# Kernel tuning notes

Hardware: AMD Instinct MI355X
Metric: run time of the kernel (lower is better)

## Reference

```python
import jax, jax.numpy as jnp
import numpy as np

B, Q, C, H, NSTEPS = 1024, 96, 16, 100, 100  # batch, q (MA order), channels, hidden, Euler steps


def setup_inputs() -> dict:
    key = jax.random.key(0)
    ks = jax.random.split(key, 6)
    s = 0.1  # weight init scale
    return {
        "series": jax.random.normal(ks[0], (B, Q, C), jnp.float32),
        "rand_error": jax.random.normal(ks[1], (B, 1, C), jnp.float32),
        "W1": jax.random.normal(ks[2], (H, Q + 2), jnp.float32) * s,
        "b1": jnp.zeros((H,), jnp.float32),
        "W2": jax.random.normal(ks[3], (H, H), jnp.float32) * s,
        "b2": jnp.zeros((H,), jnp.float32),
        "W3": jax.random.normal(ks[4], (Q + 1, H), jnp.float32) * s,
        "b3": jnp.zeros((Q + 1,), jnp.float32),
    }


def _mlp(x, t, W1, b1, W2, b2, W3, b3):
    # x: (B, Q+1, C), t: (B, 1, C)  -> cat along feature dim, permute to (B, C, Q+2)
    inp = jnp.concatenate([x, t], axis=1).transpose(0, 2, 1)
    h = jnp.tanh(inp @ W1.T + b1)
    h = jnp.tanh(h @ W2.T + b2)
    out = h @ W3.T + b3            # (B, C, Q+1)
    return out.transpose(0, 2, 1)  # (B, Q+1, C)


def reference(series, rand_error, W1, b1, W2, b2, W3, b3):
    # ma_forecast sampling path: noise = cat(series, rand_error) then Euler flow sampling
    noise = jnp.concatenate([series, rand_error], axis=1)  # (B, Q+1, C)
    dt = jnp.float32(1.0 / NSTEPS)

    def step(x, i):
        t = jnp.ones((x.shape[0], 1, x.shape[2]), x.dtype) * (i.astype(x.dtype) / NSTEPS)
        pred = _mlp(x, t, W1, b1, W2, b2, W3, b3)
        return x + (pred - noise) * dt, None

    x, _ = jax.lax.scan(step, noise, jnp.arange(NSTEPS))
    return x
```

## Files before the change

### kernel.cpp

```cpp
#include <hip/hip_runtime.h>


#define NB 1024
#define NQ 96
#define NC 16
#define NH 100
#define QP1 97
#define QP2 98
#define NTHR 256
#define STR 136
#define NSTEPS_ 100
#define MT_K 128

typedef __attribute__((ext_vector_type(8))) short bf16x8;
typedef __attribute__((ext_vector_type(4))) float f32x4;
typedef __attribute__((ext_vector_type(2))) float f32x2;
typedef __attribute__((ext_vector_type(2))) unsigned uintx2;

#define LO2(v) __builtin_shufflevector(v, v, 0, 1)
#define HI2(v) __builtin_shufflevector(v, v, 2, 3)

__device__ __forceinline__ f32x4 splat4(float f) {
  f32x4 v = f;
  return v;
}

__device__ __forceinline__ f32x2 splat2(float f) {
  f32x2 v = f;
  return v;
}

__device__ __forceinline__ short f2bf_rne(float f) {
  unsigned u = __builtin_bit_cast(unsigned, f);
  u = u + 0x7fffu + ((u >> 16) & 1u);
  return (short)(u >> 16);
}

__device__ __forceinline__ unsigned cvtpk_bf16(float a, float b) {
  unsigned r;
  asm("v_cvt_pk_bf16_f32 %0, %1, %2" : "=v"(r) : "v"(a), "v"(b));
  return r;
}

__device__ __forceinline__ void tanh_pair(f32x2& p, f32x2& q) {
  f32x2 up = p * p, uq = q * q;
  f32x2 np = p * __builtin_elementwise_fma(up + splat2(105.0f), up, splat2(945.0f));
  f32x2 nq = q * __builtin_elementwise_fma(uq + splat2(105.0f), uq, splat2(945.0f));
  f32x2 dp = __builtin_elementwise_fma(
      __builtin_elementwise_fma(splat2(15.0f), up, splat2(420.0f)), up,
      splat2(945.0f));
  f32x2 dq = __builtin_elementwise_fma(
      __builtin_elementwise_fma(splat2(15.0f), uq, splat2(420.0f)), uq,
      splat2(945.0f));
  f32x2 rp, rq;
  rp[0] = __builtin_amdgcn_rcpf(dp[0]);
  rp[1] = __builtin_amdgcn_rcpf(dp[1]);
  rq[0] = __builtin_amdgcn_rcpf(dq[0]);
  rq[1] = __builtin_amdgcn_rcpf(dq[1]);
  f32x2 vp = np * rp, vq = nq * rq;
  p = __builtin_elementwise_min(
      __builtin_elementwise_max(vp, splat2(-1.0f)), splat2(1.0f));
  q = __builtin_elementwise_min(
      __builtin_elementwise_max(vq, splat2(-1.0f)), splat2(1.0f));
}

__global__ void __launch_bounds__(512) arima_prep(
    const float* __restrict__ W1, const float* __restrict__ b1,
    const float* __restrict__ W3, const float* __restrict__ b3,
    short* __restrict__ Mt, float* __restrict__ sv) {
  __shared__ float part[4][128];
  __shared__ float pb[128];
  const int n = blockIdx.x;
  const int tid = threadIdx.x;
  const int k = tid & 127, js = tid >> 7;
  float s = 0.0f;
  if (n < NH && k < NH) {
    int j0 = js * 25, j1 = (js == 3) ? QP1 : j0 + 25;
    for (int j = j0; j < j1; ++j)
      s = fmaf(W1[n * QP2 + j], W3[j * NH + k], s);
  }
  part[js][k] = s;
  if (tid < 128)
    pb[tid] = (tid < QP1 && n < NH) ? W1[n * QP2 + tid] * b3[tid] : 0.0f;
  __syncthreads();
  if (js == 0) {
    float tot = part[0][k] + part[1][k] + part[2][k] + part[3][k];
    Mt[n * MT_K + k] = f2bf_rne(0.01f * tot);
  }
  if (tid == 0) {
    float d = 0.0f;
    for (int j = 0; j < 128; ++j) d += pb[j];
    sv[n] = (n < NH) ? 0.01f * (d + b1[n] + W1[n * QP2 + QP1]) : 0.0f;
  }
}

__device__ void load_afrag(const float* __restrict__ W,
                           const float* __restrict__ bias, int ws, int mvalid,
                           int KW, int m, int quad, bf16x8 dst[4]) {
#pragma unroll
  for (int kb = 0; kb < 4; ++kb) {
    bf16x8 v;
#pragma unroll
    for (int i = 0; i < 8; ++i) {
      int k = kb * 32 + quad * 8 + i;
      float f = 0.0f;
      if (m < mvalid) {
        if (k < KW) f = W[m * ws + k];
        else if (k == KW) f = bias[m];
      }
      v[i] = f2bf_rne(f);
    }
    dst[kb] = v;
  }
}

__device__ __forceinline__ void gemm_acc(const short* __restrict__ src,
                                         int rbase, const bf16x8 (&A)[2][4],
                                         f32x4 (&acc)[2]) {
#pragma unroll
  for (int kb = 0; kb < 4; ++kb) {
    bf16x8 bv = *(const bf16x8*)(src + rbase + kb * 32);
    acc[0] = __builtin_amdgcn_mfma_f32_16x16x32_bf16(A[0][kb], bv, acc[0], 0, 0, 0);
    acc[1] = __builtin_amdgcn_mfma_f32_16x16x32_bf16(A[1][kb], bv, acc[1], 0, 0, 0);
  }
}

__device__ __forceinline__ void write_tiles2(short* __restrict__ dst, int wrow,
                                             int T0, int quad, f32x2 a0,
                                             f32x2 a1, f32x2 b0, f32x2 b1) {
  uintx2 a, b;
  a.x = cvtpk_bf16(a0[0], a0[1]);
  a.y = cvtpk_bf16(a1[0], a1[1]);
  b.x = cvtpk_bf16(b0[0], b0[1]);
  b.y = cvtpk_bf16(b1[0], b1[1]);
  *(uintx2*)(dst + wrow + T0 * 16 + quad * 4) = a;
  *(uintx2*)(dst + wrow + (T0 + 1) * 16 + quad * 4) = b;
}

__global__ void __launch_bounds__(NTHR, 4)
arima_r15(const float* __restrict__ series,
          const float* __restrict__ rand_error, const float* __restrict__ W1,
          const float* __restrict__ b1, const float* __restrict__ W2,
          const float* __restrict__ b2, const float* __restrict__ W3,
          const float* __restrict__ b3, const short* __restrict__ Mt,
          const float* __restrict__ sv, float* __restrict__ out) {
  __shared__ __align__(16) short buf1[16 * STR];
  __shared__ __align__(16) short buf2[16 * STR];

  const int tid = threadIdx.x;
  const int w = tid >> 6, l = tid & 63;
  const int col = l & 15, quad = l >> 4;
  const int b = blockIdx.x;
  const int T0 = 2 * w;
  const int wrow = col * STR;
  const int rbase = wrow + quad * 8;
  const bool fixw = (w == 3 && quad == 1);

  {
    f32x4 xv[2];
#pragma unroll
    for (int t = 0; t < 2; ++t)
#pragma unroll
      for (int r = 0; r < 4; ++r) {
        int q = (T0 + t) * 16 + quad * 4 + r;
        float f = 0.0f;
        if (q < NQ) f = series[(b * NQ + q) * NC + col];
        else if (q == NQ) f = rand_error[b * NC + col];
        else if (q == QP2) f = 1.0f;
        xv[t][r] = f;
      }
    write_tiles2(buf2, wrow, T0, quad, LO2(xv[0]), HI2(xv[0]), LO2(xv[1]),
                 HI2(xv[1]));
  }
  __syncthreads();

  f32x4 z[2], v[2];
  {
    bf16x8 a1[2][4];
#pragma unroll
    for (int t = 0; t < 2; ++t)
      load_afrag(W1, b1, QP2, NH, QP2, (T0 + t) * 16 + col, quad, a1[t]);
    z[0] = splat4(0.0f);
    z[1] = splat4(0.0f);
    gemm_acc(buf2, rbase, a1, z);
#pragma unroll
    for (int t = 0; t < 2; ++t) {
      f32x4 s;
#pragma unroll
      for (int r = 0; r < 4; ++r) s[r] = sv[(T0 + t) * 16 + quad * 4 + r];
      v[t] = s - splat4(0.01f) * z[t];
    }
  }
  {
    f32x2 p0 = LO2(z[0]), p1 = HI2(z[0]), p2 = LO2(z[1]), p3 = HI2(z[1]);
    tanh_pair(p0, p1);
    tanh_pair(p2, p3);
    if (fixw) p0[0] = 1.0f;
    write_tiles2(buf1, wrow, T0, quad, p0, p1, p2, p3);
  }
  __syncthreads();

  bf16x8 a2[2][4], am[2][4];
#pragma unroll
  for (int t = 0; t < 2; ++t) {
    load_afrag(W2, b2, NH, NH, NH, (T0 + t) * 16 + col, quad, a2[t]);
#pragma unroll
    for (int kb = 0; kb < 4; ++kb)
      am[t][kb] = *(const bf16x8*)(Mt + ((T0 + t) * 16 + col) * MT_K +
                                   kb * 32 + quad * 8);
  }
  f32x2 h2s[2][2];
  h2s[0][0] = splat2(0.0f);
  h2s[0][1] = splat2(0.0f);
  h2s[1][0] = splat2(0.0f);
  h2s[1][1] = splat2(0.0f);

#pragma unroll 1
  for (int step = 0; step < NSTEPS_; ++step) {
    f32x4 acc[2];
    acc[0] = splat4(0.0f);
    acc[1] = splat4(0.0f);
    gemm_acc(buf1, rbase, a2, acc);
    {
      f32x2 p0 = LO2(acc[0]), p1 = HI2(acc[0]), p2 = LO2(acc[1]),
            p3 = HI2(acc[1]);
      tanh_pair(p0, p1);
      tanh_pair(p2, p3);
      write_tiles2(buf2, wrow, T0, quad, p0, p1, p2, p3);
      h2s[0][0] = h2s[0][0] + p0;
      h2s[0][1] = h2s[0][1] + p1;
      h2s[1][0] = h2s[1][0] + p2;
      h2s[1][1] = h2s[1][1] + p3;
    }
    __syncthreads();
    gemm_acc(buf2, rbase, am, z);
    {
      z[0] = z[0] + v[0];
      z[1] = z[1] + v[1];
      f32x2 q0 = LO2(z[0]), q1 = HI2(z[0]), q2 = LO2(z[1]), q3 = HI2(z[1]);
      tanh_pair(q0, q1);
      tanh_pair(q2, q3);
      if (fixw) q0[0] = 1.0f;
      write_tiles2(buf1, wrow, T0, quad, q0, q1, q2, q3);
    }
    __syncthreads();
  }

  {
    f32x2 ha00 = splat2(0.01f) * h2s[0][0];
    f32x2 ha01 = splat2(0.01f) * h2s[0][1];
    f32x2 ha10 = splat2(0.01f) * h2s[1][0];
    f32x2 ha11 = splat2(0.01f) * h2s[1][1];
    if (fixw) ha00[0] = 1.0f;
    write_tiles2(buf2, wrow, T0, quad, ha00, ha01, ha10, ha11);
  }
  __syncthreads();
  {
    bf16x8 a3[2][4];
#pragma unroll
    for (int t = 0; t < 2; ++t)
      load_afrag(W3, b3, NH, QP1, NH, (T0 + t) * 16 + col, quad, a3[t]);
    f32x4 o[2];
    o[0] = splat4(0.0f);
    o[1] = splat4(0.0f);
    gemm_acc(buf2, rbase, a3, o);
#pragma unroll
    for (int t = 0; t < 2; ++t)
#pragma unroll
      for (int r = 0; r < 4; ++r) {
        int q = (T0 + t) * 16 + quad * 4 + r;
        if (q < QP1) out[(b * QP1 + q) * NC + col] = o[t][r];
      }
  }
}

extern "C" void kernel_launch(void* const* d_in, const int* in_sizes, int n_in,
                              void* d_out, int out_size, void* d_ws,
                              size_t ws_size, hipStream_t stream) {
  const float* series = (const float*)d_in[0];
  const float* rand_error = (const float*)d_in[1];
  const float* W1 = (const float*)d_in[2];
  const float* b1 = (const float*)d_in[3];
  const float* W2 = (const float*)d_in[4];
  const float* b2 = (const float*)d_in[5];
  const float* W3 = (const float*)d_in[6];
  const float* b3 = (const float*)d_in[7];
  float* out = (float*)d_out;

  short* Mt = (short*)d_ws;
  float* sv = (float*)((char*)d_ws + MT_K * MT_K * 2);

  hipLaunchKernelGGL(arima_prep, dim3(128), dim3(512), 0, stream, W1, b1, W3,
                     b3, Mt, sv);
  hipLaunchKernelGGL(arima_r15, dim3(NB), dim3(NTHR), 0, stream, series,
                     rand_error, W1, b1, W2, b2, W3, b3, Mt, sv, out);
}
```

Before: 254.4 us.

## Process two batch elements per block to amortize barriers and weight fragments

Each block now handles two batch items with separate LDS buffers, reusing the same W2 and Mt register fragments across both and sharing one pair of __syncthreads per Euler step. The grid is halved and launch bounds are relaxed from 4 to 2 blocks per CU. This exposes independent MFMA and tanh work within a wave to hide latency and halves barrier count per item. The cost is more registers and LDS per block and fewer blocks, so there may be less parallelism across CUs (512 blocks on 256 CUs).

```diff
diff --git a/kernel.cpp b/kernel.cpp
--- a/kernel.cpp
+++ b/kernel.cpp
@@ -137,26 +137,27 @@
   *(uintx2*)(dst + wrow + (T0 + 1) * 16 + quad * 4) = b;
 }
 
-__global__ void __launch_bounds__(NTHR, 4)
-arima_r15(const float* __restrict__ series,
+__global__ void __launch_bounds__(NTHR, 2)
+arima_r17(const float* __restrict__ series,
           const float* __restrict__ rand_error, const float* __restrict__ W1,
           const float* __restrict__ b1, const float* __restrict__ W2,
           const float* __restrict__ b2, const float* __restrict__ W3,
           const float* __restrict__ b3, const short* __restrict__ Mt,
           const float* __restrict__ sv, float* __restrict__ out) {
-  __shared__ __align__(16) short buf1[16 * STR];
-  __shared__ __align__(16) short buf2[16 * STR];
+  __shared__ __align__(16) short buf1[2][16 * STR];
+  __shared__ __align__(16) short buf2[2][16 * STR];
 
   const int tid = threadIdx.x;
   const int w = tid >> 6, l = tid & 63;
   const int col = l & 15, quad = l >> 4;
-  const int b = blockIdx.x;
+  const int b0 = blockIdx.x * 2;
   const int T0 = 2 * w;
   const int wrow = col * STR;
   const int rbase = wrow + quad * 8;
   const bool fixw = (w == 3 && quad == 1);
 
-  {
+#pragma unroll
+  for (int p = 0; p < 2; ++p) {
     f32x4 xv[2];
 #pragma unroll
     for (int t = 0; t < 2; ++t)
@@ -164,39 +165,44 @@
       for (int r = 0; r < 4; ++r) {
         int q = (T0 + t) * 16 + quad * 4 + r;
         float f = 0.0f;
-        if (q < NQ) f = series[(b * NQ + q) * NC + col];
-        else if (q == NQ) f = rand_error[b * NC + col];
+        if (q < NQ) f = series[((b0 + p) * NQ + q) * NC + col];
+        else if (q == NQ) f = rand_error[(b0 + p) * NC + col];
         else if (q == QP2) f = 1.0f;
         xv[t][r] = f;
       }
-    write_tiles2(buf2, wrow, T0, quad, LO2(xv[0]), HI2(xv[0]), LO2(xv[1]),
+    write_tiles2(buf2[p], wrow, T0, quad, LO2(xv[0]), HI2(xv[0]), LO2(xv[1]),
                  HI2(xv[1]));
   }
   __syncthreads();
 
-  f32x4 z[2], v[2];
+  f32x4 z[2][2], v[2][2];
   {
     bf16x8 a1[2][4];
 #pragma unroll
     for (int t = 0; t < 2; ++t)
       load_afrag(W1, b1, QP2, NH, QP2, (T0 + t) * 16 + col, quad, a1[t]);
-    z[0] = splat4(0.0f);
-    z[1] = splat4(0.0f);
-    gemm_acc(buf2, rbase, a1, z);
-#pragma unroll
-    for (int t = 0; t < 2; ++t) {
-      f32x4 s;
-#pragma unroll
-      for (int r = 0; r < 4; ++r) s[r] = sv[(T0 + t) * 16 + quad * 4 + r];
-      v[t] = s - splat4(0.01f) * z[t];
-    }
-  }
-  {
-    f32x2 p0 = LO2(z[0]), p1 = HI2(z[0]), p2 = LO2(z[1]), p3 = HI2(z[1]);
+    f32x4 s[2];
+#pragma unroll
+    for (int t = 0; t < 2; ++t)
+#pragma unroll
+      for (int r = 0; r < 4; ++r) s[t][r] = sv[(T0 + t) * 16 + quad * 4 + r];
+#pragma unroll
+    for (int p = 0; p < 2; ++p) {
+      z[p][0] = splat4(0.0f);
+      z[p][1] = splat4(0.0f);
+      gemm_acc(buf2[p], rbase, a1, z[p]);
+#pragma unroll
+      for (int t = 0; t < 2; ++t) v[p][t] = s[t] - splat4(0.01f) * z[p][t];
+    }
+  }
+#pragma unroll
+  for (int p = 0; p < 2; ++p) {
+    f32x2 p0 = LO2(z[p][0]), p1 = HI2(z[p][0]), p2 = LO2(z[p][1]),
+          p3 = HI2(z[p][1]);
     tanh_pair(p0, p1);
     tanh_pair(p2, p3);
     if (fixw) p0[0] = 1.0f;
-    write_tiles2(buf1, wrow, T0, quad, p0, p1, p2, p3);
+    write_tiles2(buf1[p], wrow, T0, quad, p0, p1, p2, p3);
   }
   __syncthreads();
 
@@ -209,50 +215,60 @@
       am[t][kb] = *(const bf16x8*)(Mt + ((T0 + t) * 16 + col) * MT_K +
                                    kb * 32 + quad * 8);
   }
-  f32x2 h2s[2][2];
-  h2s[0][0] = splat2(0.0f);
-  h2s[0][1] = splat2(0.0f);
-  h2s[1][0] = splat2(0.0f);
-  h2s[1][1] = splat2(0.0f);
+  f32x2 h2s[2][2][2];
+#pragma unroll
+  for (int p = 0; p < 2; ++p)
+#pragma unroll
+    for (int t = 0; t < 2; ++t)
+#pragma unroll
+      for (int h = 0; h < 2; ++h) h2s[p][t][h] = splat2(0.0f);
 
 #pragma unroll 1
   for (int step = 0; step < NSTEPS_; ++step) {
-    f32x4 acc[2];
-    acc[0] = splat4(0.0f);
-    acc[1] = splat4(0.0f);
-    gemm_acc(buf1, rbase, a2, acc);
-    {
-      f32x2 p0 = LO2(acc[0]), p1 = HI2(acc[0]), p2 = LO2(acc[1]),
-            p3 = HI2(acc[1]);
+    f32x4 acc[2][2];
+#pragma unroll
+    for (int p = 0; p < 2; ++p) {
+      acc[p][0] = splat4(0.0f);
+      acc[p][1] = splat4(0.0f);
+      gemm_acc(buf1[p], rbase, a2, acc[p]);
+    }
+#pragma unroll
+    for (int p = 0; p < 2; ++p) {
+      f32x2 p0 = LO2(acc[p][0]), p1 = HI2(acc[p][0]), p2 = LO2(acc[p][1]),
+            p3 = HI2(acc[p][1]);
       tanh_pair(p0, p1);
       tanh_pair(p2, p3);
-      write_tiles2(buf2, wrow, T0, quad, p0, p1, p2, p3);
-      h2s[0][0] = h2s[0][0] + p0;
-      h2s[0][1] = h2s[0][1] + p1;
-      h2s[1][0] = h2s[1][0] + p2;
-      h2s[1][1] = h2s[1][1] + p3;
+      write_tiles2(buf2[p], wrow, T0, quad, p0, p1, p2, p3);
+      h2s[p][0][0] = h2s[p][0][0] + p0;
+      h2s[p][0][1] = h2s[p][0][1] + p1;
+      h2s[p][1][0] = h2s[p][1][0] + p2;
+      h2s[p][1][1] = h2s[p][1][1] + p3;
     }
     __syncthreads();
-    gemm_acc(buf2, rbase, am, z);
-    {
-      z[0] = z[0] + v[0];
-      z[1] = z[1] + v[1];
-      f32x2 q0 = LO2(z[0]), q1 = HI2(z[0]), q2 = LO2(z[1]), q3 = HI2(z[1]);
+#pragma unroll
+    for (int p = 0; p < 2; ++p) gemm_acc(buf2[p], rbase, am, z[p]);
+#pragma unroll
+    for (int p = 0; p < 2; ++p) {
+      z[p][0] = z[p][0] + v[p][0];
+      z[p][1] = z[p][1] + v[p][1];
+      f32x2 q0 = LO2(z[p][0]), q1 = HI2(z[p][0]), q2 = LO2(z[p][1]),
+            q3 = HI2(z[p][1]);
       tanh_pair(q0, q1);
       tanh_pair(q2, q3);
       if (fixw) q0[0] = 1.0f;
-      write_tiles2(buf1, wrow, T0, quad, q0, q1, q2, q3);
+      write_tiles2(buf1[p], wrow, T0, quad, q0, q1, q2, q3);
     }
     __syncthreads();
   }
 
-  {
-    f32x2 ha00 = splat2(0.01f) * h2s[0][0];
-    f32x2 ha01 = splat2(0.01f) * h2s[0][1];
-    f32x2 ha10 = splat2(0.01f) * h2s[1][0];
-    f32x2 ha11 = splat2(0.01f) * h2s[1][1];
+#pragma unroll
+  for (int p = 0; p < 2; ++p) {
+    f32x2 ha00 = splat2(0.01f) * h2s[p][0][0];
+    f32x2 ha01 = splat2(0.01f) * h2s[p][0][1];
+    f32x2 ha10 = splat2(0.01f) * h2s[p][1][0];
+    f32x2 ha11 = splat2(0.01f) * h2s[p][1][1];
     if (fixw) ha00[0] = 1.0f;
-    write_tiles2(buf2, wrow, T0, quad, ha00, ha01, ha10, ha11);
+    write_tiles2(buf2[p], wrow, T0, quad, ha00, ha01, ha10, ha11);
   }
   __syncthreads();
   {
@@ -260,17 +276,20 @@
 #pragma unroll
     for (int t = 0; t < 2; ++t)
       load_afrag(W3, b3, NH, QP1, NH, (T0 + t) * 16 + col, quad, a3[t]);
-    f32x4 o[2];
-    o[0] = splat4(0.0f);
-    o[1] = splat4(0.0f);
-    gemm_acc(buf2, rbase, a3, o);
-#pragma unroll
-    for (int t = 0; t < 2; ++t)
-#pragma unroll
-      for (int r = 0; r < 4; ++r) {
-        int q = (T0 + t) * 16 + quad * 4 + r;
-        if (q < QP1) out[(b * QP1 + q) * NC + col] = o[t][r];
-      }
+#pragma unroll
+    for (int p = 0; p < 2; ++p) {
+      f32x4 o[2];
+      o[0] = splat4(0.0f);
+      o[1] = splat4(0.0f);
+      gemm_acc(buf2[p], rbase, a3, o);
+#pragma unroll
+      for (int t = 0; t < 2; ++t)
+#pragma unroll
+        for (int r = 0; r < 4; ++r) {
+          int q = (T0 + t) * 16 + quad * 4 + r;
+          if (q < QP1) out[((b0 + p) * QP1 + q) * NC + col] = o[t][r];
+        }
+    }
   }
 }
 
@@ -292,6 +311,6 @@
 
   hipLaunchKernelGGL(arima_prep, dim3(128), dim3(512), 0, stream, W1, b1, W3,
                      b3, Mt, sv);
-  hipLaunchKernelGGL(arima_r15, dim3(NB), dim3(NTHR), 0, stream, series,
+  hipLaunchKernelGGL(arima_r17, dim3(NB / 2), dim3(NTHR), 0, stream, series,
                      rand_error, W1, b1, W2, b2, W3, b3, Mt, sv, out);
 }
```

New measurement: 265.6 us. 1.04x slower.
